# Kernel tuning notes

Hardware: AMD Instinct MI355X
Metric: run time of the kernel (lower is better)

Reference implementation:

```python
import jax, jax.numpy as jnp
import numpy as np

N_FFT = 512
HOP = 128
SR = 16000
N_MELS = N_FFT // 2 + 1  # 257, per __init__ (n_mels = n_fft//2+1)
EPS, S, ALPHA, DELTA, R = 1e-6, 0.025, 0.98, 2.0, 0.5  # pcenfunc defaults


def _mel_fbanks():
    # torchaudio melscale_fbanks with mel_scale='htk', norm=None, f_min=0, f_max=sr/2
    n_freqs = N_FFT // 2 + 1
    all_freqs = np.linspace(0.0, SR / 2.0, n_freqs)
    hz2mel = lambda f: 2595.0 * np.log10(1.0 + f / 700.0)
    mel2hz = lambda m: 700.0 * (10.0 ** (m / 2595.0) - 1.0)
    m_pts = np.linspace(hz2mel(0.0), hz2mel(SR / 2.0), N_MELS + 2)
    f_pts = mel2hz(m_pts)
    f_diff = f_pts[1:] - f_pts[:-1]
    slopes = f_pts[None, :] - all_freqs[:, None]  # (n_freqs, n_mels+2)
    down = -slopes[:, :-2] / f_diff[:-1]
    up = slopes[:, 2:] / f_diff[1:]
    fb = np.maximum(0.0, np.minimum(down, up))  # (n_freqs, n_mels)
    return jnp.asarray(fb, jnp.float32)


def _stft(sig, window):
    # torch.stft: center=True, reflect pad, win_length=n_fft, onesided
    pad = N_FFT // 2
    xp = jnp.pad(sig, (pad, pad), mode='reflect')
    n_frames = 1 + (xp.shape[0] - N_FFT) // HOP
    idx = jnp.arange(n_frames)[:, None] * HOP + jnp.arange(N_FFT)[None, :]
    frames = xp[idx] * window  # (frames, n_fft)
    return jnp.fft.rfft(frames, axis=-1)  # (frames, freq)


def _unwrap_time(p):
    # np.unwrap along the frames axis (axis=0 here since layout is (frames, freq))
    dd = jnp.diff(p, axis=0)
    ddmod = jnp.mod(dd + jnp.pi, 2.0 * jnp.pi) - jnp.pi
    ddmod = jnp.where((ddmod == -jnp.pi) & (dd > 0), jnp.pi, ddmod)
    corr = jnp.where(jnp.abs(dd) < jnp.pi, 0.0, ddmod - dd)
    return p + jnp.pad(jnp.cumsum(corr, axis=0), ((1, 0), (0, 0)))


def _pcen(x):
    # x: (frames, n_mels); m_0 = s*x_0, m_t = (1-s)*m_{t-1} + s*x_t
    m0 = S * x[0]
    def step(m, xt):
        m = (1.0 - S) * m + S * xt
        return m, m
    _, ms = jax.lax.scan(step, m0, x[1:])
    M = jnp.concatenate([m0[None], ms], axis=0)
    return (x / (M + EPS) ** ALPHA + DELTA) ** R - DELTA ** R


def setup_inputs() -> dict:
    key = jax.random.key(0)
    T = 4_800_000  # 5 minutes @ 16 kHz -> frames = 37501
    audio = jax.random.normal(key, (1, T), dtype=jnp.float32)
    return {"audio": audio, "mel_fbanks": _mel_fbanks()}


def reference(audio, mel_fbanks):
    sig = audio[0]  # batch of 1, as in the original (squeeze/unsqueeze)
    # torch.stft with window=None uses a rectangular (ones) window
    spec = _stft(sig, jnp.ones((N_FFT,), jnp.float32))  # (frames, freq) complex
    log_mag = jnp.log(jnp.abs(spec) + 1e-9)  # (frames, freq)
    # demodulated phase (on-device unwrap replaces the CPU round-trip)
    phase = _unwrap_time(jnp.angle(spec))
    real_demod = jnp.sin(phase)
    imag_demod = jnp.cos(phase)
    # MelSpectrogram: hann (periodic) window, power=2
    n = jnp.arange(N_FFT)
    hann = (0.5 * (1.0 - jnp.cos(2.0 * jnp.pi * n / N_FFT))).astype(jnp.float32)
    mspec = jnp.abs(_stft(sig, hann)) ** 2  # (frames, freq)
    mel = mspec @ mel_fbanks  # (frames, n_mels)
    pcen = _pcen(mel)  # (frames, n_mels); n_mels == freq here
    # perm(2,0,1) on (1, freq, frames) then cat along dim 1 -> (frames, 4, freq)
    data = jnp.stack([log_mag, pcen, real_demod, imag_demod], axis=1)
    # F.normalize(data, dim=0): L2 over the frames axis, eps=1e-12
    norm = jnp.maximum(jnp.linalg.norm(data, axis=0, keepdims=True), 1e-12)
    return data / norm
```

## Files before the change

### kernel.cpp

```cpp
#include <hip/hip_runtime.h>
#include <math.h>

#define NFFT 512
#define HOP 128
#define NBINS 257
#define ROW 1028
#define CHUNK 64
#define LAM64 0.19783147f
#define SWZ(a) ((a) ^ (((a) >> 4) & 15))

__device__ __forceinline__ float2 cmul(float2 a, float2 b) {
  return make_float2(a.x * b.x - a.y * b.y, a.x * b.y + a.y * b.x);
}

struct EB { float lg, sv, cv, msp; };

__global__ void k_prep(const float* __restrict__ fb, int* __restrict__ lohi,
                       float2* __restrict__ twg) {
  int t = threadIdx.x;
  for (int i = t; i < NFFT; i += 256) {
    double ang = -6.283185307179586476925286766559 * (double)i / (double)NFFT;
    twg[i] = make_float2((float)cos(ang), (float)sin(ang));
  }
  for (int m = t; m < NBINS; m += 256) {
    int lo = 0, hi = -1;
    for (int f = 0; f < NBINS; ++f) {
      if (fb[f * NBINS + m] != 0.0f) { if (hi < 0) lo = f; hi = f; }
    }
    lohi[m] = lo;
    lohi[NBINS + m] = hi;
  }
}

__device__ __forceinline__ EB epilogue_bin(const float2* __restrict__ S, int off,
                                           float* __restrict__ out, unsigned ob,
                                           int k, bool store) {
  float2 z = S[SWZ(off + k)];
  float mag, sv, cv;
  if (k == 0 || k == 256) {
    mag = fabsf(z.x);
    sv = sinf(atan2f(0.0f, z.x));
    cv = copysignf(1.0f, z.x);
  } else {
    float r2 = fmaf(z.x, z.x, z.y * z.y);
    if (r2 > 0.0f) {
      float rs = __builtin_amdgcn_rsqf(r2);
      mag = r2 * rs;
      sv = z.y * rs;
      cv = z.x * rs;
    } else { mag = 0.0f; sv = 0.0f; cv = 1.0f; }
  }
  float lg = __logf(mag + 1e-9f);
  if (store) {
    out[ob + k] = lg;
    out[ob + 2 * NBINS + k] = sv;
    out[ob + 3 * NBINS + k] = cv;
  }
  float2 zm, zp;
  if (k == 0) { float2 s1 = S[SWZ(off + 1)]; zm = make_float2(s1.x, -s1.y); }
  else zm = S[SWZ(off + k - 1)];
  zp = S[SWZ(off + k + 1)];
  float hr = 0.5f * z.x - 0.25f * (zm.x + zp.x);
  float hi = 0.5f * z.y - 0.25f * (zm.y + zp.y);
  EB e; e.lg = lg; e.sv = sv; e.cv = cv; e.msp = hr * hr + hi * hi;
  return e;
}

__global__ __launch_bounds__(256) void k_fft(
    const float* __restrict__ audio, const float* __restrict__ fb,
    const int* __restrict__ lohi, const float2* __restrict__ twg,
    float* __restrict__ out, float* __restrict__ partF, int T, int nframes) {
  __shared__ float2 bufA[2][520];
  __shared__ float2 bufB[2][520];

  const int t = threadIdx.x;
  const int ff = t >> 7;
  const int v = t & 127;
  const int frb = blockIdx.x * 4;
  const int fr0 = frb + 2 * ff;
  const int fr1 = fr0 + 1;
  const bool h0 = fr0 < nframes;
  const bool h1 = fr1 < nframes;

  float2* __restrict__ xa = bufA[ff];
  float2* __restrict__ xb = bufB[ff];

  int s0 = fr0 * HOP - NFFT / 2;
  float2 xr[4];
#pragma unroll
  for (int j = 0; j < 4; ++j) {
    int i = v + 128 * j;
    int q0 = s0 + i;
    if (q0 < 0) q0 = -q0;
    if (q0 >= T) q0 = 2 * T - 2 - q0;
    int q1 = s0 + HOP + i;
    if (q1 < 0) q1 = -q1;
    if (q1 >= T) q1 = 2 * T - 2 - q1;
    xr[j] = make_float2(audio[q0], h1 ? audio[q1] : 0.0f);
  }
  {
    float2 w1 = twg[v], w2 = twg[2 * v], w3 = twg[3 * v];
    float2 s02 = make_float2(xr[0].x + xr[2].x, xr[0].y + xr[2].y);
    float2 d02 = make_float2(xr[0].x - xr[2].x, xr[0].y - xr[2].y);
    float2 s13 = make_float2(xr[1].x + xr[3].x, xr[1].y + xr[3].y);
    float2 d13 = make_float2(xr[1].x - xr[3].x, xr[1].y - xr[3].y);
    int o = 4 * v;
    xb[SWZ(o)] = make_float2(s02.x + s13.x, s02.y + s13.y);
    xb[SWZ(o + 1)] = cmul(w1, make_float2(d02.x + d13.y, d02.y - d13.x));
    xb[SWZ(o + 2)] = cmul(w2, make_float2(s02.x - s13.x, s02.y - s13.y));
    xb[SWZ(o + 3)] = cmul(w3, make_float2(d02.x - d13.y, d02.y + d13.x));
  }
  __syncthreads();

  const int ra0 = SWZ(v), ra1 = SWZ(v + 128), ra2 = SWZ(v + 256), ra3 = SWZ(v + 384);
  float2* x = xb;
  float2* y = xa;
#pragma unroll
  for (int ds = 1; ds < 4; ++ds) {
    const int m = 1 << (2 * ds);
    int qm = v & ~(m - 1);
    int r = v - qm;
    int o = 4 * qm + r;
    float2 w1 = twg[qm];
    float2 w2 = twg[2 * qm];
    float2 w3 = twg[3 * qm];
    float2 x0 = x[ra0], x1 = x[ra1], x2 = x[ra2], x3 = x[ra3];
    float2 s02 = make_float2(x0.x + x2.x, x0.y + x2.y);
    float2 d02 = make_float2(x0.x - x2.x, x0.y - x2.y);
    float2 s13 = make_float2(x1.x + x3.x, x1.y + x3.y);
    float2 d13 = make_float2(x1.x - x3.x, x1.y - x3.y);
    float2 E0 = make_float2(s02.x + s13.x, s02.y + s13.y);
    float2 u1 = make_float2(d02.x + d13.y, d02.y - d13.x);
    float2 u2 = make_float2(s02.x - s13.x, s02.y - s13.y);
    float2 u3 = make_float2(d02.x - d13.y, d02.y + d13.x);
    float2 E1 = cmul(w1, u1);
    float2 E2 = cmul(w2, u2);
    float2 E3 = cmul(w3, u3);
    y[SWZ(o)] = E0;
    y[SWZ(o + m)] = E1;
    y[SWZ(o + 2 * m)] = E2;
    y[SWZ(o + 3 * m)] = E3;
    __syncthreads();
    float2* tmp = x; x = y; y = tmp;
  }
  for (int k = v; k < 258; k += 128) {
    float2 Zk, Zm;
    if (k <= 255) {
      float2 a0 = x[SWZ(k)], a1 = x[SWZ(k + 256)];
      Zk = make_float2(a0.x + a1.x, a0.y + a1.y);
    } else {
      float2 a0 = x[SWZ(k - 256)], a1 = x[SWZ(k)];
      Zk = make_float2(a0.x - a1.x, a0.y - a1.y);
    }
    int m2 = (NFFT - k) & (NFFT - 1);
    if (k == 0 || k == 256) {
      Zm = Zk;
    } else if (m2 >= 256) {
      float2 b0 = x[SWZ(m2 - 256)], b1 = x[SWZ(m2)];
      Zm = make_float2(b0.x - b1.x, b0.y - b1.y);
    } else {
      float2 b0 = x[SWZ(m2)], b1 = x[SWZ(m2 + 256)];
      Zm = make_float2(b0.x + b1.x, b0.y + b1.y);
    }
    y[SWZ(k)] = make_float2(0.5f * (Zk.x + Zm.x), 0.5f * (Zk.y - Zm.y));
    y[SWZ(258 + k)] = make_float2(0.5f * (Zk.y + Zm.y), 0.5f * (Zm.x - Zk.x));
  }
  __syncthreads();

  unsigned ob0 = (unsigned)fr0 * ROW;
  unsigned ob1 = (unsigned)fr1 * ROW;
  float mspA[3], mspB[3], sql[3], sqs[3], sqc[3];
#pragma unroll
  for (int ki = 0; ki < 3; ++ki) {
    int k = v + 128 * ki;
    if (k <= 256) {
      EB e0 = epilogue_bin(y, 0, out, ob0, k, h0);
      EB e1 = epilogue_bin(y, 258, out, ob1, k, h1);
      mspA[ki] = e0.msp;
      mspB[ki] = e1.msp;
      sql[ki] = (h0 ? e0.lg * e0.lg : 0.f) + (h1 ? e1.lg * e1.lg : 0.f);
      sqs[ki] = (h0 ? e0.sv * e0.sv : 0.f) + (h1 ? e1.sv * e1.sv : 0.f);
      sqc[ki] = (h0 ? e0.cv * e0.cv : 0.f) + (h1 ? e1.cv * e1.cv : 0.f);
    }
  }
  __syncthreads();

  float* mspSh = (float*)&bufB[ff][0];
  float* sqf = (float*)&bufA[ff][0];
#pragma unroll
  for (int ki = 0; ki < 3; ++ki) {
    int k = v + 128 * ki;
    if (k <= 256) {
      mspSh[k] = mspA[ki];
      mspSh[258 + k] = mspB[ki];
      sqf[k] = sql[ki];
      sqf[258 + k] = sqs[ki];
      sqf[516 + k] = sqc[ki];
    }
  }
  __syncthreads();

  for (int m = v; m < NBINS; m += 128) {
    int lo = lohi[m], hi = lohi[NBINS + m];
    float a0 = 0.0f, a1 = 0.0f;
    for (int f = lo; f <= hi; ++f) {
      float w = fb[f * NBINS + m];
      a0 = fmaf(mspSh[f], w, a0);
      a1 = fmaf(mspSh[258 + f], w, a1);
    }
    if (h0) out[ob0 + NBINS + m] = a0;
    if (h1) out[ob1 + NBINS + m] = a1;
  }

  const float* sq0 = (const float*)&bufA[0][0];
  const float* sq1 = (const float*)&bufA[1][0];
  for (int i = t; i < 771; i += 256) {
    int lidx = i + (i >= 257) + (i >= 514);
    partF[(unsigned)blockIdx.x * 771u + i] = sq0[lidx] + sq1[lidx];
  }
}

__global__ __launch_bounds__(320) void k_pcen_a(const float* __restrict__ out,
                                                float* __restrict__ mend, int nframes) {
  int m = threadIdx.x;
  if (m >= NBINS) return;
  int c = blockIdx.x;
  int F0 = c * CHUNK;
  int end = min(F0 + CHUNK, nframes);
  const float SS = 0.025f, OMS = 1.0f - SS;
  float mm = 0.0f;
  int tf = F0;
  for (; tf + 16 <= end; tf += 16) {
    float xs[16];
#pragma unroll
    for (int j = 0; j < 16; ++j) xs[j] = out[(unsigned)(tf + j) * ROW + NBINS + m];
#pragma unroll
    for (int j = 0; j < 16; ++j) mm = OMS * mm + SS * xs[j];
  }
  for (; tf < end; ++tf) mm = OMS * mm + SS * out[(unsigned)tf * ROW + NBINS + m];
  mend[c * NBINS + m] = mm;
}

__global__ __launch_bounds__(320) void k_pcen_c(float* __restrict__ out,
                                                const float* __restrict__ mend,
                                                float* __restrict__ partC,
                                                int nframes) {
  int m = threadIdx.x;
  if (m >= NBINS) return;
  int c = blockIdx.x;
  int F0 = c * CHUNK;
  int end = min(F0 + CHUNK, nframes);
  const float SS = 0.025f, OMS = 1.0f - SS;
  const float SQ2 = sqrtf(2.0f);
  float mm;
  if (c >= 12) {
    float xs[12];
#pragma unroll
    for (int j = 0; j < 12; ++j) xs[j] = mend[(c - 12 + j) * NBINS + m];
    mm = 0.0f;
#pragma unroll
    for (int j = 0; j < 12; ++j) mm = xs[j] + LAM64 * mm;
  } else {
    mm = 0.0f;
    for (int j = 0; j < c; ++j) mm = mend[j * NBINS + m] + LAM64 * mm;
  }
  float acc1 = 0.0f;
  int tf = F0;
  for (; tf + 16 <= end; tf += 16) {
    float xs[16], ys[16];
#pragma unroll
    for (int j = 0; j < 16; ++j) xs[j] = out[(unsigned)(tf + j) * ROW + NBINS + m];
#pragma unroll
    for (int j = 0; j < 16; ++j) {
      mm = OMS * mm + SS * xs[j];
      float invden = __expf(-0.98f * __logf(mm + 1e-6f));
      float val = fmaf(xs[j], invden, 2.0f);
      float rs = __builtin_amdgcn_rsqf(val);
      ys[j] = val * rs - SQ2;
      acc1 = fmaf(ys[j], ys[j], acc1);
    }
#pragma unroll
    for (int j = 0; j < 16; ++j) out[(unsigned)(tf + j) * ROW + NBINS + m] = ys[j];
  }
  for (; tf < end; ++tf) {
    unsigned idx = (unsigned)tf * ROW + NBINS + m;
    float xv = out[idx];
    mm = OMS * mm + SS * xv;
    float invden = __expf(-0.98f * __logf(mm + 1e-6f));
    float val = fmaf(xv, invden, 2.0f);
    float rs = __builtin_amdgcn_rsqf(val);
    float yv = val * rs - SQ2;
    acc1 = fmaf(yv, yv, acc1);
    out[idx] = yv;
  }
  partC[c * NBINS + m] = acc1;
}

__global__ __launch_bounds__(256) void k_norm(const float* __restrict__ partF,
                                              const float* __restrict__ partC,
                                              float* __restrict__ invn,
                                              int nfb, int chunks) {
  __shared__ float red[256];
  int c = blockIdx.x, t = threadIdx.x;
  float s = 0.0f;
  if (c >= 257 && c < 514) {
    int m = c - 257;
    for (int r = t; r < chunks; r += 256) s += partC[r * NBINS + m];
  } else {
    int i = (c < 257) ? c : c - 257;
    for (int r = t; r < nfb; r += 256) s += partF[(unsigned)r * 771u + i];
  }
  red[t] = s;
  __syncthreads();
  for (int o = 128; o > 0; o >>= 1) {
    if (t < o) red[t] += red[t + o];
    __syncthreads();
  }
  if (t == 0) invn[c] = 1.0f / fmaxf(sqrtf(red[0]), 1e-12f);
}

__global__ __launch_bounds__(256) void k_scale(float4* __restrict__ out4,
                                               const float* __restrict__ invn,
                                               long n4) {
  __shared__ float inv[ROW];
  for (int i = threadIdx.x; i < ROW; i += 256) inv[i] = invn[i];
  __syncthreads();
  long stride = (long)gridDim.x * 256;
  for (long i = (long)blockIdx.x * 256 + threadIdx.x; i < n4; i += stride) {
    float4 v = out4[i];
    int col = (int)((i * 4) % ROW);
    v.x *= inv[col];
    v.y *= inv[col + 1];
    v.z *= inv[col + 2];
    v.w *= inv[col + 3];
    out4[i] = v;
  }
}

extern "C" void kernel_launch(void* const* d_in, const int* in_sizes, int n_in,
                              void* d_out, int out_size, void* d_ws, size_t ws_size,
                              hipStream_t stream) {
  const float* audio = (const float*)d_in[0];
  const float* fb = (const float*)d_in[1];
  int T = in_sizes[0];
  int nframes = 1 + T / HOP;
  float* out = (float*)d_out;
  int chunks = (nframes + CHUNK - 1) / CHUNK;
  int nfb = (nframes + 3) / 4;

  float* wsf = (float*)d_ws;
  float2* twg = (float2*)wsf;
  float* mend = wsf + 1024;
  float* invn = mend + (long)chunks * NBINS;
  int* lohi = (int*)(invn + ROW);
  float* partC = (float*)(lohi + 2 * NBINS);
  float* partF = partC + (long)chunks * NBINS;

  k_prep<<<1, 256, 0, stream>>>(fb, lohi, twg);
  k_fft<<<nfb, 256, 0, stream>>>(audio, fb, lohi, twg, out, partF, T, nframes);
  k_pcen_a<<<chunks, 320, 0, stream>>>(out, mend, nframes);
  k_pcen_c<<<chunks, 320, 0, stream>>>(out, mend, partC, nframes);
  k_norm<<<ROW, 256, 0, stream>>>(partF, partC, invn, nfb, chunks);
  long n4 = (long)nframes * ROW / 4;
  k_scale<<<2048, 256, 0, stream>>>((float4*)out, invn, n4);
}
```

Baseline: 214.5 us.

## Split column-norm reduction into coalesced two-stage passes and simplify scale indexing

The old norm kernel gave each column its own block, so every block read one strided element per row of the partial sums. The new k_norm1 instead assigns row groups to 40 blocks, each reading whole contiguous rows, and a tiny k_norm2 finishes the column sums. The scale kernel now maps each thread to a fixed float4 column within a frame, which removes the per-element modulo and the shared-memory table. The costs are one more kernel launch and idle lanes in the 320-thread scale blocks, since only 257 of them do work.

```diff
diff --git a/kernel.cpp b/kernel.cpp
--- a/kernel.cpp
+++ b/kernel.cpp
@@ -296,44 +296,73 @@
   partC[c * NBINS + m] = acc1;
 }
 
-__global__ __launch_bounds__(256) void k_norm(const float* __restrict__ partF,
-                                              const float* __restrict__ partC,
-                                              float* __restrict__ invn,
-                                              int nfb, int chunks) {
-  __shared__ float red[256];
-  int c = blockIdx.x, t = threadIdx.x;
+__global__ __launch_bounds__(256) void k_norm1(const float* __restrict__ partF,
+                                               const float* __restrict__ partC,
+                                               float* __restrict__ part2F,
+                                               float* __restrict__ part2C,
+                                               int nfb, int chunks) {
+  int t = threadIdx.x;
+  if (blockIdx.x < 32) {
+    int rg = blockIdx.x;
+    int per = (nfb + 31) / 32;
+    int r0 = rg * per, r1 = min(r0 + per, nfb);
+    float a0 = 0.f, a1 = 0.f, a2 = 0.f, a3 = 0.f;
+    for (int r = r0; r < r1; ++r) {
+      unsigned base = (unsigned)r * 771u;
+      a0 += partF[base + t];
+      a1 += partF[base + t + 256];
+      if (t + 512 < 771) a2 += partF[base + t + 512];
+      if (t < 3) a3 += partF[base + t + 768];
+    }
+    part2F[rg * 771 + t] = a0;
+    part2F[rg * 771 + t + 256] = a1;
+    if (t + 512 < 771) part2F[rg * 771 + t + 512] = a2;
+    if (t < 3) part2F[rg * 771 + t + 768] = a3;
+  } else {
+    int rg = blockIdx.x - 32;
+    int per = (chunks + 7) / 8;
+    int r0 = rg * per, r1 = min(r0 + per, chunks);
+    float a0 = 0.f, a1 = 0.f;
+    for (int r = r0; r < r1; ++r) {
+      unsigned base = (unsigned)r * 257u;
+      a0 += partC[base + t];
+      if (t == 0) a1 += partC[base + 256];
+    }
+    part2C[rg * 257 + t] = a0;
+    if (t == 0) part2C[rg * 257 + 256] = a1;
+  }
+}
+
+__global__ __launch_bounds__(256) void k_norm2(const float* __restrict__ part2F,
+                                               const float* __restrict__ part2C,
+                                               float* __restrict__ invn) {
+  int c = blockIdx.x * 256 + threadIdx.x;
+  if (c >= ROW) return;
   float s = 0.0f;
   if (c >= 257 && c < 514) {
     int m = c - 257;
-    for (int r = t; r < chunks; r += 256) s += partC[r * NBINS + m];
+    for (int g = 0; g < 8; ++g) s += part2C[g * 257 + m];
   } else {
     int i = (c < 257) ? c : c - 257;
-    for (int r = t; r < nfb; r += 256) s += partF[(unsigned)r * 771u + i];
-  }
-  red[t] = s;
-  __syncthreads();
-  for (int o = 128; o > 0; o >>= 1) {
-    if (t < o) red[t] += red[t + o];
-    __syncthreads();
-  }
-  if (t == 0) invn[c] = 1.0f / fmaxf(sqrtf(red[0]), 1e-12f);
-}
-
-__global__ __launch_bounds__(256) void k_scale(float4* __restrict__ out4,
+    for (int g = 0; g < 32; ++g) s += part2F[g * 771 + i];
+  }
+  invn[c] = 1.0f / fmaxf(sqrtf(s), 1e-12f);
+}
+
+__global__ __launch_bounds__(320) void k_scale(float4* __restrict__ out4,
                                                const float* __restrict__ invn,
-                                               long n4) {
-  __shared__ float inv[ROW];
-  for (int i = threadIdx.x; i < ROW; i += 256) inv[i] = invn[i];
-  __syncthreads();
-  long stride = (long)gridDim.x * 256;
-  for (long i = (long)blockIdx.x * 256 + threadIdx.x; i < n4; i += stride) {
-    float4 v = out4[i];
-    int col = (int)((i * 4) % ROW);
-    v.x *= inv[col];
-    v.y *= inv[col + 1];
-    v.z *= inv[col + 2];
-    v.w *= inv[col + 3];
-    out4[i] = v;
+                                               int nframes) {
+  int t = threadIdx.x;
+  if (t >= 257) return;
+  float4 iv = make_float4(invn[4 * t], invn[4 * t + 1], invn[4 * t + 2], invn[4 * t + 3]);
+  for (unsigned fr = blockIdx.x; fr < (unsigned)nframes; fr += gridDim.x) {
+    unsigned idx = fr * 257u + t;
+    float4 v = out4[idx];
+    v.x *= iv.x;
+    v.y *= iv.y;
+    v.z *= iv.z;
+    v.w *= iv.w;
+    out4[idx] = v;
   }
 }
 
@@ -354,13 +383,15 @@
   float* invn = mend + (long)chunks * NBINS;
   int* lohi = (int*)(invn + ROW);
   float* partC = (float*)(lohi + 2 * NBINS);
-  float* partF = partC + (long)chunks * NBINS;
+  float* part2F = partC + (long)chunks * NBINS;
+  float* part2C = part2F + 32 * 771;
+  float* partF = part2C + 8 * 257;
 
   k_prep<<<1, 256, 0, stream>>>(fb, lohi, twg);
   k_fft<<<nfb, 256, 0, stream>>>(audio, fb, lohi, twg, out, partF, T, nframes);
   k_pcen_a<<<chunks, 320, 0, stream>>>(out, mend, nframes);
   k_pcen_c<<<chunks, 320, 0, stream>>>(out, mend, partC, nframes);
-  k_norm<<<ROW, 256, 0, stream>>>(partF, partC, invn, nfb, chunks);
-  long n4 = (long)nframes * ROW / 4;
-  k_scale<<<2048, 256, 0, stream>>>((float4*)out, invn, n4);
-}
+  k_norm1<<<40, 256, 0, stream>>>(partF, partC, part2F, part2C, nfb, chunks);
+  k_norm2<<<(ROW + 255) / 256, 256, 0, stream>>>(part2F, part2C, invn);
+  k_scale<<<2048, 320, 0, stream>>>((float4*)out, invn, nframes);
+}
```

Result: slower. 317.7 us (+48.1%).
